# Optimization experiments

Hardware: AMD Instinct MI355X
Metric: run time of the kernel (lower is better)

Reference implementation:

```python
import math
import jax, jax.numpy as jnp
import numpy as np

# ---- static configuration (mirrors init_kwargs / chosen shapes) ----
MUL = 16          # multiplicity in "16x0e+16x1e+16x2e"
B_CFG = 64        # number of configurations in batch
N_ATOM = 64       # atoms per configuration
N_NODES = B_CFG * N_ATOM
N_PAIRS = B_CFG * N_ATOM * N_ATOM

# ---- real Wigner 3j symbols (e3nn convention), computed once in numpy ----
def _su2_cg(j1, m1, j2, m2, j3, m3):
    if m3 != m1 + m2:
        return 0.0
    f = math.factorial
    vmin = max(-j1 + j2 + m3, -j1 + m1, 0)
    vmax = min(j2 + j3 + m1, j3 - j1 + j2, j3 + m3)
    C = math.sqrt((2 * j3 + 1) * f(j3 + j1 - j2) * f(j3 - j1 + j2) * f(j1 + j2 - j3)
                  * f(j3 + m3) * f(j3 - m3)
                  / (f(j1 + j2 + j3 + 1) * f(j1 - m1) * f(j1 + m1) * f(j2 - m2) * f(j2 + m2)))
    S = 0.0
    for v in range(vmin, vmax + 1):
        S += (-1) ** (v + j2 + m2) * f(j2 + j3 + m1 - v) * f(j1 - m1 + v) / (
            f(v) * f(j3 - j1 + j2 - v) * f(j3 + m3 - v) * f(v + j1 - j2 - m3))
    return C * S

def _q_real_to_complex(l):
    q = np.zeros((2 * l + 1, 2 * l + 1), dtype=np.complex128)
    for m in range(-l, 0):
        q[l + m, l + abs(m)] = 1 / 2 ** 0.5
        q[l + m, l - abs(m)] = -1j / 2 ** 0.5
    q[l, l] = 1.0
    for m in range(1, l + 1):
        q[l + m, l + abs(m)] = (-1) ** m / 2 ** 0.5
        q[l + m, l - abs(m)] = 1j * (-1) ** m / 2 ** 0.5
    return (-1j) ** l * q

def _wigner_3j(l1, l2, l3):
    C = np.zeros((2 * l1 + 1, 2 * l2 + 1, 2 * l3 + 1))
    for m1 in range(-l1, l1 + 1):
        for m2 in range(-l2, l2 + 1):
            m3 = m1 + m2
            if abs(m3) <= l3:
                C[l1 + m1, l2 + m2, l3 + m3] = _su2_cg(l1, m1, l2, m2, l3, m3)
    Q1, Q2, Q3 = _q_real_to_complex(l1), _q_real_to_complex(l2), _q_real_to_complex(l3)
    Cr = np.einsum('ij,kl,mn,ikm->jln', Q1, Q2, np.conj(Q3), C.astype(np.complex128))
    assert np.abs(Cr.imag).max() < 1e-6
    Cr = Cr.real
    return Cr / np.linalg.norm(Cr)

# all CG paths (l1, l2, l_out) of the fully connected TP (0e+1e+2e)^2 -> 0e+1e+2e
PATHS = [(0, 0, 0), (1, 1, 0), (2, 2, 0),
         (0, 1, 1), (1, 0, 1), (1, 1, 1), (1, 2, 1), (2, 1, 1), (2, 2, 1),
         (0, 2, 2), (2, 0, 2), (1, 1, 2), (1, 2, 2), (2, 1, 2), (2, 2, 2)]
W3J = {p: _wigner_3j(*p) for p in set(PATHS)}
FAN = {lo: sum(1 for p in PATHS if p[2] == lo) * MUL * MUL for lo in (0, 1, 2)}
ALPHA = {lo: math.sqrt(2 * lo + 1) / math.sqrt(FAN[lo]) for lo in (0, 1, 2)}
# CartesianTensor('ij=ij') change of basis: x_ij = sum_{l,m} QCART[lm,i,j] * irreps[lm]
QCART = np.concatenate([math.sqrt(2 * l + 1) * np.transpose(_wigner_3j(1, 1, l), (2, 0, 1))
                        for l in (0, 1, 2)], axis=0)  # (9, 3, 3), orthonormal rows


def setup_inputs() -> dict:
    key = jax.random.key(0)
    k1, k2 = jax.random.split(key)
    node_feats = jax.random.normal(k1, (N_NODES, MUL * 9), dtype=jnp.float32)
    # layout: for each config, all (i, j) atom pairs with global node indices
    ii, jj = jnp.meshgrid(jnp.arange(N_ATOM, dtype=jnp.int32),
                          jnp.arange(N_ATOM, dtype=jnp.int32), indexing='ij')
    base = (jnp.arange(B_CFG, dtype=jnp.int32) * N_ATOM)[:, None, None]
    rows = (base + ii[None]).reshape(-1)
    cols = (base + jj[None]).reshape(-1)
    layout = jnp.stack([rows, cols], axis=1)  # (N_PAIRS, 2) int32
    tp_weights = jax.random.normal(k2, (len(PATHS), MUL, MUL), dtype=jnp.float32)
    return {'node_feats': node_feats, 'layout': layout, 'tp_weights': tp_weights}


def _split(x):
    # (E, MUL*9) -> {l: (E, MUL, 2l+1)} in irreps order 16x0e | 16x1e | 16x2e
    E = x.shape[0]
    return {0: x[:, :MUL].reshape(E, MUL, 1),
            1: x[:, MUL:4 * MUL].reshape(E, MUL, 3),
            2: x[:, 4 * MUL:].reshape(E, MUL, 5)}


def _forward(node_feats, tp_weights, layout):
    x1 = _split(node_feats[layout[:, 0]])   # gather row atoms
    x2 = _split(node_feats[layout[:, 1]])   # gather column atoms
    E = layout.shape[0]
    dt = node_feats.dtype
    out = {lo: jnp.zeros((E, 2 * lo + 1), dt) for lo in (0, 1, 2)}
    for p, (l1, l2, lo) in enumerate(PATHS):
        w3j = jnp.asarray(W3J[(l1, l2, lo)], dt)
        t = jnp.einsum('eui,uv->evi', x1[l1], tp_weights[p])          # mix multiplicities
        out[lo] = out[lo] + ALPHA[lo] * jnp.einsum('evi,evj,ijk->ek', t, x2[l2], w3j)
    irr = jnp.concatenate([out[0], out[1], out[2]], axis=1)           # (E, 9) = 0e+1e+2e
    cart = jnp.einsum('ek,kij->eij', irr, jnp.asarray(QCART, dt))     # (E, 3, 3)
    # symmetrize: (H + H^T)/2 on the 3n x 3n per-config Hessian
    c = cart.reshape(B_CFG, N_ATOM, N_ATOM, 3, 3)
    c = 0.5 * (c + jnp.transpose(c, (0, 2, 1, 4, 3)))
    return c.reshape(E, 3, 3)


def reference(node_feats, layout, tp_weights):
    return _forward(node_feats, tp_weights, layout)
```

## Files before the change

### kernel.cpp

```cpp
#include <hip/hip_runtime.h>
#include <math.h>


#define NPATH 15

constexpr double cfact(int n){ double r = 1.0; for (int i = 2; i <= n; ++i) r *= (double)i; return r; }
constexpr double csqrt(double x){
  if (x <= 0.0) return 0.0;
  double g = x < 1.0 ? 1.0 : x;
  for (int i = 0; i < 64; ++i) g = 0.5*(g + x/g);
  return g;
}

constexpr double ccg(int j1,int m1,int j2,int m2,int j3,int m3){
  if (m3 != m1 + m2) return 0.0;
  int vmin = -j1 + j2 + m3;
  if (-j1 + m1 > vmin) vmin = -j1 + m1;
  if (0 > vmin) vmin = 0;
  int vmax = j2 + j3 + m1;
  if (j3 - j1 + j2 < vmax) vmax = j3 - j1 + j2;
  if (j3 + m3 < vmax) vmax = j3 + m3;
  double C = csqrt((2.0*j3+1.0)*cfact(j3+j1-j2)*cfact(j3-j1+j2)*cfact(j1+j2-j3)
                   *cfact(j3+m3)*cfact(j3-m3)
                   /(cfact(j1+j2+j3+1)*cfact(j1-m1)*cfact(j1+m1)*cfact(j2-m2)*cfact(j2+m2)));
  double S = 0.0;
  for (int v = vmin; v <= vmax; ++v){
    double term = cfact(j2+j3+m1-v)*cfact(j1-m1+v)
                /(cfact(v)*cfact(j3-j1+j2-v)*cfact(j3+m3-v)*cfact(v+j1-j2-m3));
    S += ((v + j2 + m2) & 1) ? -term : term;
  }
  return C * S;
}

struct QM { double re[5][5]; double im[5][5]; };
constexpr QM cbuild_q(int l){
  QM q{};
  double s = 1.0 / csqrt(2.0);
  for (int m = -l; m < 0; ++m){
    q.re[l+m][l-m] = s;
    q.im[l+m][l+m] = -s;
  }
  q.re[l][l] = 1.0;
  for (int m = 1; m <= l; ++m){
    double sg = (m & 1) ? -1.0 : 1.0;
    q.re[l+m][l+m] = sg * s;
    q.im[l+m][l-m] = sg * s;
  }
  if (l == 1){
    for (int r = 0; r < 5; ++r)
      for (int c = 0; c < 5; ++c){
        double a = q.re[r][c], b = q.im[r][c];
        q.re[r][c] = b; q.im[r][c] = -a;
      }
  } else if (l == 2){
    for (int r = 0; r < 5; ++r)
      for (int c = 0; c < 5; ++c){ q.re[r][c] = -q.re[r][c]; q.im[r][c] = -q.im[r][c]; }
  }
  return q;
}

struct CRP { double v[125]; };
constexpr CRP make_cr(int l1, int l2, int l3){
  QM q1 = cbuild_q(l1), q2 = cbuild_q(l2), q3 = cbuild_q(l3);
  const int d1 = 2*l1+1, d2 = 2*l2+1, d3 = 2*l3+1;
  double CG[125] = {};
  for (int i = 0; i < d1; ++i)
    for (int k = 0; k < d2; ++k)
      for (int m = 0; m < d3; ++m)
        CG[(i*5 + k)*5 + m] = ccg(l1, i-l1, l2, k-l2, l3, m-l3);
  CRP o{};
  for (int j = 0; j < d1; ++j)
    for (int l = 0; l < d2; ++l)
      for (int n = 0; n < d3; ++n){
        double acc = 0.0;
        for (int i = 0; i < d1; ++i)
          for (int k = 0; k < d2; ++k)
            for (int m = 0; m < d3; ++m){
              double c = CG[(i*5 + k)*5 + m];
              if (c == 0.0) continue;
              double are = q1.re[i][j], aim = q1.im[i][j];
              double bre = q2.re[k][l], bim = q2.im[k][l];
              double tre = are*bre - aim*bim;
              double tim = are*bim + aim*bre;
              double cre = q3.re[m][n], cim = q3.im[m][n];
              acc += (tre*cre + tim*cim) * c;
            }
        o.v[(j*d2 + l)*d3 + n] = acc;
      }
  double s2 = 0.0;
  for (int e = 0; e < d1*d2*d3; ++e) s2 += o.v[e]*o.v[e];
  double inv = 1.0 / csqrt(s2);
  for (int e = 0; e < d1*d2*d3; ++e) o.v[e] *= inv;
  return o;
}

constexpr CRP CR0  = make_cr(0,0,0);
constexpr CRP CR1  = make_cr(1,1,0);
constexpr CRP CR2  = make_cr(2,2,0);
constexpr CRP CR3  = make_cr(0,1,1);
constexpr CRP CR4  = make_cr(1,0,1);
constexpr CRP CR5  = make_cr(1,1,1);
constexpr CRP CR6  = make_cr(1,2,1);
constexpr CRP CR7  = make_cr(2,1,1);
constexpr CRP CR8  = make_cr(2,2,1);
constexpr CRP CR9  = make_cr(0,2,2);
constexpr CRP CR10 = make_cr(2,0,2);
constexpr CRP CR11 = make_cr(1,1,2);
constexpr CRP CR12 = make_cr(1,2,2);
constexpr CRP CR13 = make_cr(2,1,2);
constexpr CRP CR14 = make_cr(2,2,2);

struct QCT { double v[81]; };
constexpr QCT make_qc(){
  QCT q{};
  for (int lm = 0; lm < 9; ++lm){
    int l = (lm == 0) ? 0 : ((lm < 4) ? 1 : 2);
    int m = lm - l*l;
    const CRP& cr = (l == 0) ? CR1 : ((l == 1) ? CR5 : CR11);
    double sc = csqrt(2.0*l + 1.0);
    for (int r = 0; r < 9; ++r)
      q.v[lm*9 + r] = cr.v[r*(2*l+1) + m] * sc;
  }
  return q;
}
constexpr QCT QCt = make_qc();

struct WQT { float b8[189*8]; float b1[189]; };
constexpr WQT make_wq(){
  WQT t{};
  const CRP* crs[NPATH] = {&CR0,&CR1,&CR2,&CR3,&CR4,&CR5,&CR6,&CR7,&CR8,&CR9,
                           &CR10,&CR11,&CR12,&CR13,&CR14};
  const int L1[NPATH]   = {0,1,2,0,1,1,1,2,2,0,2,1,1,2,2};
  const int L2[NPATH]   = {0,1,2,1,0,1,2,1,2,2,0,1,2,1,2};
  const int LO[NPATH]   = {0,0,0,1,1,1,1,1,1,2,2,2,2,2,2};
  const int PROW[NPATH] = {0,1,10,35,38,41,50,65,80,105,110,115,124,139,164};
  const double AL[3] = { csqrt(1.0/768.0), csqrt(3.0/1536.0), csqrt(5.0/1536.0) };
  for (int p = 0; p < NPATH; ++p){
    const int d1 = 2*L1[p]+1, d2 = 2*L2[p]+1, d3 = 2*LO[p]+1, lo = LO[p];
    for (int i = 0; i < d1; ++i)
      for (int j = 0; j < d2; ++j)
        for (int a = 0; a < 9; ++a){
          double acc = 0.0;
          for (int m = 0; m < d3; ++m)
            acc += crs[p]->v[(i*d2 + j)*d3 + m] * QCt.v[(lo*lo + m)*9 + a];
          double val = AL[lo] * acc;
          int row = PROW[p] + i*d2 + j;
          if (a < 8) t.b8[row*8 + a] = (float)val;
          else       t.b1[row]       = (float)val;
        }
  }
  return t;
}
__constant__ WQT cWQ = make_wq();

__constant__ int cP_L1[NPATH]   = {0,1,2,0,1,1,1,2,2,0,2,1,1,2,2};
__constant__ int cC2P[51] = {0, 1,1,1, 2,2,2,2,2, 3, 4,4,4, 5,5,5, 6,6,6,
                             7,7,7,7,7, 8,8,8,8,8, 9, 10,10,10,10,10,
                             11,11,11, 12,12,12, 13,13,13,13,13, 14,14,14,14,14};
__constant__ int cC2I[51] = {0, 0,1,2, 0,1,2,3,4, 0, 0,1,2, 0,1,2, 0,1,2,
                             0,1,2,3,4, 0,1,2,3,4, 0, 0,1,2,3,4,
                             0,1,2, 0,1,2, 0,1,2,3,4, 0,1,2,3,4};

#define ACCP(TOFF_, PROW_, D1_)                                              \
  { _Pragma("unroll")                                                        \
    for (int i = 0; i < (D1_); ++i){                                         \
      float tv = pT[((TOFF_) + i) * 16 + v];                                 \
      int row = (PROW_) + i * D2 + j;                                        \
      const float4 m0 = *(const float4*)&sB8[row * 8];                       \
      const float4 m1 = *(const float4*)&sB8[row * 8 + 4];                   \
      const float  m8 = sB1[row];                                            \
      acc[0] += tv*m0.x; acc[1] += tv*m0.y; acc[2] += tv*m0.z;               \
      acc[3] += tv*m0.w; acc[4] += tv*m1.x; acc[5] += tv*m1.y;               \
      acc[6] += tv*m1.z; acc[7] += tv*m1.w; acc[8] += tv*m8;                 \
    } }

__global__ __launch_bounds__(256, 2) void fused2_kernel(
    const float* __restrict__ feats,
    const int*   __restrict__ layout,
    const float* __restrict__ tpw,
    float*       __restrict__ out)
{
  __shared__ __align__(16) float U[11664];
  __shared__ __align__(16) float sMq[4][1728];
  __shared__ __align__(16) float sX1[4][144];
  __shared__ int sCol[64];

  const int tid  = threadIdx.x;
  const int wave = tid >> 6;
  const int lane = tid & 63;
  const int rwBase = blockIdx.x * 4;

  float* sB8  = U;
  float* sB1  = U + 1512;
  float* sTPW = U + 4968;

  for (int o = tid; o < 1512; o += 256) sB8[o] = cWQ.b8[o];
  if (tid < 189) sB1[tid] = cWQ.b1[tid];
  for (int q = tid; q < 960; q += 256)
    *(float4*)&sTPW[q * 4] = ((const float4*)tpw)[q];
  if (tid < 144){
    int w = tid / 36, q = tid - w * 36;
    int rn = layout[2 * ((rwBase + w) * 64)];
    *(float4*)&sX1[w][q * 4] = *(const float4*)(feats + (size_t)rn * 144 + q * 4);
  }
  if (tid >= 192)
    sCol[tid - 192] = layout[2 * ((size_t)rwBase * 64 + (tid - 192)) + 1];
  __syncthreads();

  float* pT = U + 1704 + wave * 816;
  {
    const int v  = lane & 15;
    const int cq = lane >> 4;
    const float* xw = sX1[wave];
    for (int it = 0; it < 13; ++it){
      int c = cq + it * 4;
      if (c < 51){
        int p = cC2P[c], i = cC2I[c];
        int l1 = cP_L1[p];
        int st = 2 * l1 + 1;
        int loff = (l1 == 0) ? 0 : ((l1 == 1) ? 16 : 64);
        const float* xb = xw + loff + i;
        const float* wb = sTPW + p * 256 + v;
        float s = 0.f;
        #pragma unroll
        for (int u = 0; u < 16; ++u) s += xb[u * st] * wb[u * 16];
        pT[c * 16 + v] = s;
      }
    }
  }

  float* pM = sMq[wave];
  for (int rnd = 0; rnd < 3; ++rnd){
    int c = lane + rnd * 64;
    if (c >= 144) break;
    float acc[9];
    #pragma unroll
    for (int a = 0; a < 9; ++a) acc[a] = 0.f;
    if (c < 16){
      const int v = c, j = 0;
      const int D2 = 1;
      ACCP(0,  0,   1)
      ACCP(10, 38,  3)
      ACCP(30, 110, 5)
    } else if (c < 64){
      const int v = (c - 16) / 3, j = (c - 16) % 3;
      const int D2 = 3;
      ACCP(1,  1,   3)
      ACCP(9,  35,  1)
      ACCP(13, 41,  3)
      ACCP(19, 65,  5)
      ACCP(35, 115, 3)
      ACCP(41, 139, 5)
    } else {
      const int v = (c - 64) / 5, j = (c - 64) % 5;
      const int D2 = 5;
      ACCP(4,  10,  5)
      ACCP(16, 50,  3)
      ACCP(24, 80,  5)
      ACCP(29, 105, 1)
      ACCP(38, 124, 3)
      ACCP(46, 164, 5)
    }
    *(float4*)&pM[c * 12]     = make_float4(acc[0], acc[1], acc[2], acc[3]);
    *(float4*)&pM[c * 12 + 4] = make_float4(acc[4], acc[5], acc[6], acc[7]);
    pM[c * 12 + 8] = acc[8];
  }
  __syncthreads();

  float* sX2T = U;
  #pragma unroll
  for (int k = 0; k < 9; ++k){
    int q = k * 256 + tid;
    int j = q / 36, c4 = q - j * 36;
    const float4 xv = *(const float4*)(feats + (size_t)sCol[j] * 144 + c4 * 4);
    int c0 = c4 * 4;
    sX2T[(c0 + 0) * 65 + j] = xv.x;
    sX2T[(c0 + 1) * 65 + j] = xv.y;
    sX2T[(c0 + 2) * 65 + j] = xv.z;
    sX2T[(c0 + 3) * 65 + j] = xv.w;
  }
  __syncthreads();

  float acc[9];
  #pragma unroll
  for (int a = 0; a < 9; ++a) acc[a] = 0.f;

  #pragma unroll 8
  for (int c = 0; c < 144; ++c){
    float x = sX2T[c * 65 + lane];
    const float4 m0 = *(const float4*)&pM[c * 12];
    const float4 m1 = *(const float4*)&pM[c * 12 + 4];
    const float  m8 = pM[c * 12 + 8];
    acc[0] += x * m0.x; acc[1] += x * m0.y; acc[2] += x * m0.z;
    acc[3] += x * m0.w; acc[4] += x * m1.x; acc[5] += x * m1.y;
    acc[6] += x * m1.z; acc[7] += x * m1.w; acc[8] += x * m8;
  }

  float* pO = U + 9360 + wave * 576;
  #pragma unroll
  for (int a = 0; a < 9; ++a) pO[lane * 9 + a] = acc[a];
  float* ob = out + (size_t)(rwBase + wave) * 576;
  #pragma unroll
  for (int r = 0; r < 3; ++r){
    int idx = lane + r * 64;
    if (idx < 144){
      float4 vv = *(const float4*)(pO + idx * 4);
      *(float4*)(ob + idx * 4) = vv;
    }
  }
}

__global__ __launch_bounds__(256) void sym_tiled(float* __restrict__ out){
  __shared__ float sA[16 * 145];
  __shared__ float sB[16 * 145];
  const int tid = threadIdx.x;
  const int b  = blockIdx.x / 10;
  const int tp = blockIdx.x - b * 10;
  const int TI[10] = {0,0,0,0,1,1,1,2,2,3};
  const int TJ[10] = {0,1,2,3,1,2,3,2,3,3};
  const int ti = TI[tp], tj = TJ[tp];
  const bool diag = (ti == tj);
  const size_t cfgBase = (size_t)b * 4096 * 9;

  for (int idx = tid; idx < 2304; idx += 256){
    int r = idx / 144, off = idx - r * 144;
    sA[r * 145 + off] = out[cfgBase + ((size_t)(ti*16 + r) * 64 + tj*16) * 9 + off];
  }
  if (!diag){
    for (int idx = tid; idx < 2304; idx += 256){
      int r = idx / 144, off = idx - r * 144;
      sB[r * 145 + off] = out[cfgBase + ((size_t)(tj*16 + r) * 64 + ti*16) * 9 + off];
    }
  }
  __syncthreads();

  const int di = tid >> 4, dj = tid & 15;
  const float* A = sA;
  const float* B = diag ? sA : sB;
  float oa[9], ob[9];
  #pragma unroll
  for (int a = 0; a < 3; ++a)
    #pragma unroll
    for (int d = 0; d < 3; ++d){
      oa[a*3+d] = 0.5f * (A[di*145 + dj*9 + a*3+d] + B[dj*145 + di*9 + d*3+a]);
      if (!diag)
        ob[a*3+d] = 0.5f * (B[di*145 + dj*9 + a*3+d] + A[dj*145 + di*9 + d*3+a]);
    }
  __syncthreads();

  #pragma unroll
  for (int r9 = 0; r9 < 9; ++r9) sA[di*145 + dj*9 + r9] = oa[r9];
  if (!diag){
    #pragma unroll
    for (int r9 = 0; r9 < 9; ++r9) sB[di*145 + dj*9 + r9] = ob[r9];
  }
  __syncthreads();

  for (int idx = tid; idx < 2304; idx += 256){
    int r = idx / 144, off = idx - r * 144;
    out[cfgBase + ((size_t)(ti*16 + r) * 64 + tj*16) * 9 + off] = sA[r * 145 + off];
  }
  if (!diag){
    for (int idx = tid; idx < 2304; idx += 256){
      int r = idx / 144, off = idx - r * 144;
      out[cfgBase + ((size_t)(tj*16 + r) * 64 + ti*16) * 9 + off] = sB[r * 145 + off];
    }
  }
}

extern "C" void kernel_launch(void* const* d_in, const int* in_sizes, int n_in,
                              void* d_out, int out_size, void* d_ws, size_t ws_size,
                              hipStream_t stream) {
  const float* feats  = (const float*)d_in[0];
  const int*   layout = (const int*)  d_in[1];
  const float* tpw    = (const float*)d_in[2];
  float* out = (float*)d_out;
  (void)d_ws; (void)ws_size; (void)n_in; (void)out_size;

  const int E = in_sizes[1] / 2;
  const int R = E / 64;
  const int B = E / 4096;

  fused2_kernel<<<R / 4, 256, 0, stream>>>(feats, layout, tpw, out);
  sym_tiled<<<B * 10, 256, 0, stream>>>(out);
}
```

Before: 112.5 us.

## Keep per-row Mq in registers, broadcast via readlane, swizzle X2 layout

The per-row contraction matrix Mq is now kept in registers, three chunks per lane, and broadcast across the wave with readlane. It is no longer staged in a per-wave shared-memory buffer. X2 is stored row-major with an XOR swizzle and read as float4 instead of a padded transposed layout. TP weights and X1 are pre-transposed, so the first contraction uses float4 loads and a precomputed metadata table, and occupancy is raised to 3 blocks per SM. This cuts LDS footprint and traffic, but adds many scalar readlane operations and more register pressure.

```diff
diff --git a/kernel.cpp b/kernel.cpp
--- a/kernel.cpp
+++ b/kernel.cpp
@@ -174,132 +174,167 @@
       acc[6] += tv*m1.z; acc[7] += tv*m1.w; acc[8] += tv*m8;                 \
     } }
 
-__global__ __launch_bounds__(256, 2) void fused2_kernel(
+__device__ __forceinline__ void mqc(int c, const float* pT, const float* sB8,
+                                    const float* sB1, float (&acc)[9]){
+  #pragma unroll
+  for (int a = 0; a < 9; ++a) acc[a] = 0.f;
+  if (c < 16){
+    const int v = c, j = 0;
+    const int D2 = 1;
+    ACCP(0,  0,   1)
+    ACCP(10, 38,  3)
+    ACCP(30, 110, 5)
+  } else if (c < 64){
+    const int v = (c - 16) / 3, j = (c - 16) % 3;
+    const int D2 = 3;
+    ACCP(1,  1,   3)
+    ACCP(9,  35,  1)
+    ACCP(13, 41,  3)
+    ACCP(19, 65,  5)
+    ACCP(35, 115, 3)
+    ACCP(41, 139, 5)
+  } else {
+    const int v = (c - 64) / 5, j = (c - 64) % 5;
+    const int D2 = 5;
+    ACCP(4,  10,  5)
+    ACCP(16, 50,  3)
+    ACCP(24, 80,  5)
+    ACCP(29, 105, 1)
+    ACCP(38, 124, 3)
+    ACCP(46, 164, 5)
+  }
+}
+
+__device__ __forceinline__ float rlane(float x, int l){
+  return __int_as_float(__builtin_amdgcn_readlane(__float_as_int(x), l));
+}
+
+#define CCHUNK(MQ_, BASE_) {                                                 \
+  float4 xv = *(const float4*)(xrow + ((c4 ^ lswz) << 2));                   \
+  int l0 = c4 * 4 - (BASE_);                                                 \
+  _Pragma("unroll")                                                          \
+  for (int r = 0; r < 4; ++r){                                               \
+    float xs = (r == 0) ? xv.x : ((r == 1) ? xv.y : ((r == 2) ? xv.z : xv.w)); \
+    acc[0] += xs * rlane(MQ_[0], l0 + r);                                    \
+    acc[1] += xs * rlane(MQ_[1], l0 + r);                                    \
+    acc[2] += xs * rlane(MQ_[2], l0 + r);                                    \
+    acc[3] += xs * rlane(MQ_[3], l0 + r);                                    \
+    acc[4] += xs * rlane(MQ_[4], l0 + r);                                    \
+    acc[5] += xs * rlane(MQ_[5], l0 + r);                                    \
+    acc[6] += xs * rlane(MQ_[6], l0 + r);                                    \
+    acc[7] += xs * rlane(MQ_[7], l0 + r);                                    \
+    acc[8] += xs * rlane(MQ_[8], l0 + r);                                    \
+  } }
+
+__global__ __launch_bounds__(256, 3) void fused3_kernel(
     const float* __restrict__ feats,
     const int*   __restrict__ layout,
     const float* __restrict__ tpw,
     float*       __restrict__ out)
 {
-  __shared__ __align__(16) float U[11664];
-  __shared__ __align__(16) float sMq[4][1728];
-  __shared__ __align__(16) float sX1[4][144];
+  __shared__ __align__(16) float U[11520];
+  __shared__ __align__(16) float sX1T[4][192];
   __shared__ int sCol[64];
+  __shared__ int sMeta[51];
 
   const int tid  = threadIdx.x;
   const int wave = tid >> 6;
   const int lane = tid & 63;
   const int rwBase = blockIdx.x * 4;
-
-  float* sB8  = U;
-  float* sB1  = U + 1512;
-  float* sTPW = U + 4968;
+  const int rw = rwBase + wave;
+
+  float* sB8   = U;
+  float* sB1   = U + 1512;
+  float* sTPWT = U + 4968;
 
   for (int o = tid; o < 1512; o += 256) sB8[o] = cWQ.b8[o];
   if (tid < 189) sB1[tid] = cWQ.b1[tid];
-  for (int q = tid; q < 960; q += 256)
-    *(float4*)&sTPW[q * 4] = ((const float4*)tpw)[q];
-  if (tid < 144){
-    int w = tid / 36, q = tid - w * 36;
-    int rn = layout[2 * ((rwBase + w) * 64)];
-    *(float4*)&sX1[w][q * 4] = *(const float4*)(feats + (size_t)rn * 144 + q * 4);
+  for (int e = tid; e < 3840; e += 256){
+    int p = e >> 8, r = e & 255, u = r >> 4, v = r & 15;
+    sTPWT[p * 324 + v * 20 + u] = tpw[e];
+  }
+  if (tid < 51){
+    int p = cC2P[tid], i = cC2I[tid], l1 = cP_L1[p];
+    int xb = (l1 == 0) ? 0 : ((l1 == 1) ? 16 + i * 20 : 80 + i * 20);
+    sMeta[tid] = xb | ((p * 324) << 16);
   }
   if (tid >= 192)
     sCol[tid - 192] = layout[2 * ((size_t)rwBase * 64 + (tid - 192)) + 1];
+
+  {
+    int rn = layout[2 * (rw * 64)];
+    rn = __builtin_amdgcn_readfirstlane(rn);
+    const float* g = feats + (size_t)rn * 144;
+    float* xt = sX1T[wave];
+    if (lane < 16) xt[lane] = g[lane];
+    if (lane < 48){ int i = lane >> 4, u = lane & 15;
+      xt[16 + i * 20 + u] = g[16 + u * 3 + i]; }
+    { int i = lane >> 4, u = lane & 15;
+      xt[80 + i * 20 + u] = g[64 + u * 5 + i]; }
+    if (lane < 16) xt[160 + lane] = g[64 + lane * 5 + 4];
+  }
   __syncthreads();
 
   float* pT = U + 1704 + wave * 816;
   {
     const int v  = lane & 15;
     const int cq = lane >> 4;
-    const float* xw = sX1[wave];
+    const float* xw = sX1T[wave];
+    #pragma unroll
     for (int it = 0; it < 13; ++it){
       int c = cq + it * 4;
       if (c < 51){
-        int p = cC2P[c], i = cC2I[c];
-        int l1 = cP_L1[p];
-        int st = 2 * l1 + 1;
-        int loff = (l1 == 0) ? 0 : ((l1 == 1) ? 16 : 64);
-        const float* xb = xw + loff + i;
-        const float* wb = sTPW + p * 256 + v;
+        int md = sMeta[c];
+        const float* xb = xw + (md & 0xffff);
+        const float* wb = sTPWT + (md >> 16) + v * 20;
         float s = 0.f;
         #pragma unroll
-        for (int u = 0; u < 16; ++u) s += xb[u * st] * wb[u * 16];
+        for (int u4 = 0; u4 < 4; ++u4){
+          float4 xv = *(const float4*)(xb + u4 * 4);
+          float4 wv = *(const float4*)(wb + u4 * 4);
+          s += xv.x * wv.x; s += xv.y * wv.y;
+          s += xv.z * wv.z; s += xv.w * wv.w;
+        }
         pT[c * 16 + v] = s;
       }
     }
   }
 
-  float* pM = sMq[wave];
-  for (int rnd = 0; rnd < 3; ++rnd){
-    int c = lane + rnd * 64;
-    if (c >= 144) break;
-    float acc[9];
-    #pragma unroll
-    for (int a = 0; a < 9; ++a) acc[a] = 0.f;
-    if (c < 16){
-      const int v = c, j = 0;
-      const int D2 = 1;
-      ACCP(0,  0,   1)
-      ACCP(10, 38,  3)
-      ACCP(30, 110, 5)
-    } else if (c < 64){
-      const int v = (c - 16) / 3, j = (c - 16) % 3;
-      const int D2 = 3;
-      ACCP(1,  1,   3)
-      ACCP(9,  35,  1)
-      ACCP(13, 41,  3)
-      ACCP(19, 65,  5)
-      ACCP(35, 115, 3)
-      ACCP(41, 139, 5)
-    } else {
-      const int v = (c - 64) / 5, j = (c - 64) % 5;
-      const int D2 = 5;
-      ACCP(4,  10,  5)
-      ACCP(16, 50,  3)
-      ACCP(24, 80,  5)
-      ACCP(29, 105, 1)
-      ACCP(38, 124, 3)
-      ACCP(46, 164, 5)
-    }
-    *(float4*)&pM[c * 12]     = make_float4(acc[0], acc[1], acc[2], acc[3]);
-    *(float4*)&pM[c * 12 + 4] = make_float4(acc[4], acc[5], acc[6], acc[7]);
-    pM[c * 12 + 8] = acc[8];
-  }
-  __syncthreads();
-
-  float* sX2T = U;
+  float mq0[9], mq1[9], mq2[9];
+  #pragma unroll
+  for (int a = 0; a < 9; ++a) mq2[a] = 0.f;
+  mqc(lane,       pT, sB8, sB1, mq0);
+  mqc(lane + 64,  pT, sB8, sB1, mq1);
+  if (lane < 16) mqc(lane + 128, pT, sB8, sB1, mq2);
+  __syncthreads();
+
+  float* sX2 = U;
   #pragma unroll
   for (int k = 0; k < 9; ++k){
     int q = k * 256 + tid;
     int j = q / 36, c4 = q - j * 36;
     const float4 xv = *(const float4*)(feats + (size_t)sCol[j] * 144 + c4 * 4);
-    int c0 = c4 * 4;
-    sX2T[(c0 + 0) * 65 + j] = xv.x;
-    sX2T[(c0 + 1) * 65 + j] = xv.y;
-    sX2T[(c0 + 2) * 65 + j] = xv.z;
-    sX2T[(c0 + 3) * 65 + j] = xv.w;
-  }
-  __syncthreads();
-
+    *(float4*)(sX2 + j * 144 + ((c4 ^ (j & 3)) << 2)) = xv;
+  }
+  __syncthreads();
+
+  const float* xrow = sX2 + lane * 144;
+  const int lswz = lane & 3;
   float acc[9];
   #pragma unroll
   for (int a = 0; a < 9; ++a) acc[a] = 0.f;
 
-  #pragma unroll 8
-  for (int c = 0; c < 144; ++c){
-    float x = sX2T[c * 65 + lane];
-    const float4 m0 = *(const float4*)&pM[c * 12];
-    const float4 m1 = *(const float4*)&pM[c * 12 + 4];
-    const float  m8 = pM[c * 12 + 8];
-    acc[0] += x * m0.x; acc[1] += x * m0.y; acc[2] += x * m0.z;
-    acc[3] += x * m0.w; acc[4] += x * m1.x; acc[5] += x * m1.y;
-    acc[6] += x * m1.z; acc[7] += x * m1.w; acc[8] += x * m8;
-  }
-
-  float* pO = U + 9360 + wave * 576;
+  #pragma unroll 2
+  for (int c4 = 0; c4 < 16; ++c4) CCHUNK(mq0, 0)
+  #pragma unroll 2
+  for (int c4 = 16; c4 < 32; ++c4) CCHUNK(mq1, 64)
+  #pragma unroll 2
+  for (int c4 = 32; c4 < 36; ++c4) CCHUNK(mq2, 128)
+
+  float* pO = U + 9216 + wave * 576;
   #pragma unroll
   for (int a = 0; a < 9; ++a) pO[lane * 9 + a] = acc[a];
-  float* ob = out + (size_t)(rwBase + wave) * 576;
+  float* ob = out + (size_t)rw * 576;
   #pragma unroll
   for (int r = 0; r < 3; ++r){
     int idx = lane + r * 64;
@@ -381,6 +416,6 @@
   const int R = E / 64;
   const int B = E / 4096;
 
-  fused2_kernel<<<R / 4, 256, 0, stream>>>(feats, layout, tpw, out);
+  fused3_kernel<<<R / 4, 256, 0, stream>>>(feats, layout, tpw, out);
   sym_tiled<<<B * 10, 256, 0, stream>>>(out);
 }
```

New measurement: 165.9 us. 1.47x slower.

## Stage per-row contraction matrix in global workspace to cut LDS and raise occupancy

Applied to the files above, without the earlier changes.

Adds a new fused kernel that writes each row's 144x9 contraction matrix to a global workspace instead of shared memory, then reads it back through the cache during the final contraction. It also transposes the TP weights and row features in shared memory for float4 dot products, and XOR-swizzles the gathered column features to avoid bank conflicts. The smaller LDS footprint allows three blocks per CU instead of two. The cost is extra global write and read traffic for the matrix, and the old kernel remains as a fallback when the workspace is too small.

```diff
diff --git a/kernel.cpp b/kernel.cpp
--- a/kernel.cpp
+++ b/kernel.cpp
@@ -3,6 +3,8 @@
 
 
 #define NPATH 15
+#define MQ_ROW 12
+#define MQ_STRIDE (144 * MQ_ROW)
 
 constexpr double cfact(int n){ double r = 1.0; for (int i = 2; i <= n; ++i) r *= (double)i; return r; }
 constexpr double csqrt(double x){
@@ -174,6 +176,169 @@
       acc[6] += tv*m1.z; acc[7] += tv*m1.w; acc[8] += tv*m8;                 \
     } }
 
+__global__ __launch_bounds__(256, 3) void fused4_kernel(
+    const float* __restrict__ feats,
+    const int*   __restrict__ layout,
+    const float* __restrict__ tpw,
+    float*       __restrict__ mqg,
+    float*       __restrict__ out)
+{
+  __shared__ __align__(16) float U[11520];
+  __shared__ __align__(16) float sX1T[4][192];
+  __shared__ int sCol[64];
+  __shared__ int sMeta[51];
+
+  const int tid  = threadIdx.x;
+  const int wave = tid >> 6;
+  const int lane = tid & 63;
+  const int rwBase = blockIdx.x * 4;
+  const int rw = rwBase + wave;
+
+  float* sB8   = U;
+  float* sB1   = U + 1512;
+  float* sTPWT = U + 4968;
+
+  for (int o = tid; o < 1512; o += 256) sB8[o] = cWQ.b8[o];
+  if (tid < 189) sB1[tid] = cWQ.b1[tid];
+  for (int e = tid; e < 3840; e += 256){
+    int p = e >> 8, r = e & 255, u = r >> 4, v = r & 15;
+    sTPWT[p * 324 + v * 20 + u] = tpw[e];
+  }
+  if (tid < 51){
+    int p = cC2P[tid], i = cC2I[tid], l1 = cP_L1[p];
+    int xb = (l1 == 0) ? 0 : ((l1 == 1) ? 16 + i * 20 : 80 + i * 20);
+    sMeta[tid] = xb | ((p * 324) << 16);
+  }
+  if (tid >= 192)
+    sCol[tid - 192] = layout[2 * ((size_t)rwBase * 64 + (tid - 192)) + 1];
+
+  {
+    int rn = layout[2 * (rw * 64)];
+    rn = __builtin_amdgcn_readfirstlane(rn);
+    const float* g = feats + (size_t)rn * 144;
+    float* xt = sX1T[wave];
+    if (lane < 16) xt[lane] = g[lane];
+    if (lane < 48){ int i = lane >> 4, u = lane & 15;
+      xt[16 + i * 20 + u] = g[16 + u * 3 + i]; }
+    { int i = lane >> 4, u = lane & 15;
+      xt[80 + i * 20 + u] = g[64 + u * 5 + i]; }
+    if (lane < 16) xt[160 + lane] = g[64 + lane * 5 + 4];
+  }
+  __syncthreads();
+
+  float* pT = U + 1704 + wave * 816;
+  {
+    const int v  = lane & 15;
+    const int cq = lane >> 4;
+    const float* xw = sX1T[wave];
+    #pragma unroll
+    for (int it = 0; it < 13; ++it){
+      int c = cq + it * 4;
+      if (c < 51){
+        int md = sMeta[c];
+        const float* xb = xw + (md & 0xffff);
+        const float* wb = sTPWT + (md >> 16) + v * 20;
+        float s = 0.f;
+        #pragma unroll
+        for (int u4 = 0; u4 < 4; ++u4){
+          float4 xv = *(const float4*)(xb + u4 * 4);
+          float4 wv = *(const float4*)(wb + u4 * 4);
+          s += xv.x * wv.x; s += xv.y * wv.y;
+          s += xv.z * wv.z; s += xv.w * wv.w;
+        }
+        pT[c * 16 + v] = s;
+      }
+    }
+  }
+
+  {
+    float* __restrict__ mqw = mqg + (size_t)rw * MQ_STRIDE;
+    for (int rnd = 0; rnd < 3; ++rnd){
+      int c = lane + rnd * 64;
+      if (c >= 144) break;
+      float acc[9];
+      #pragma unroll
+      for (int a = 0; a < 9; ++a) acc[a] = 0.f;
+      if (c < 16){
+        const int v = c, j = 0;
+        const int D2 = 1;
+        ACCP(0,  0,   1)
+        ACCP(10, 38,  3)
+        ACCP(30, 110, 5)
+      } else if (c < 64){
+        const int v = (c - 16) / 3, j = (c - 16) % 3;
+        const int D2 = 3;
+        ACCP(1,  1,   3)
+        ACCP(9,  35,  1)
+        ACCP(13, 41,  3)
+        ACCP(19, 65,  5)
+        ACCP(35, 115, 3)
+        ACCP(41, 139, 5)
+      } else {
+        const int v = (c - 64) / 5, j = (c - 64) % 5;
+        const int D2 = 5;
+        ACCP(4,  10,  5)
+        ACCP(16, 50,  3)
+        ACCP(24, 80,  5)
+        ACCP(29, 105, 1)
+        ACCP(38, 124, 3)
+        ACCP(46, 164, 5)
+      }
+      *(float4*)(mqw + c * MQ_ROW)     = make_float4(acc[0], acc[1], acc[2], acc[3]);
+      *(float4*)(mqw + c * MQ_ROW + 4) = make_float4(acc[4], acc[5], acc[6], acc[7]);
+      mqw[c * MQ_ROW + 8] = acc[8];
+    }
+  }
+  __syncthreads();
+
+  float* sX2 = U;
+  #pragma unroll
+  for (int k = 0; k < 9; ++k){
+    int q = k * 256 + tid;
+    int j = q / 36, c4 = q - j * 36;
+    const float4 xv = *(const float4*)(feats + (size_t)sCol[j] * 144 + c4 * 4);
+    *(float4*)(sX2 + j * 144 + ((c4 ^ (j & 3)) << 2)) = xv;
+  }
+  __syncthreads();
+
+  const float* mqr = mqg + (size_t)rw * MQ_STRIDE;
+  asm volatile("" : "+v"(mqr));
+  const float* xrow = sX2 + lane * 144;
+  const int lswz = lane & 3;
+  float acc[9];
+  #pragma unroll
+  for (int a = 0; a < 9; ++a) acc[a] = 0.f;
+
+  #pragma unroll 4
+  for (int c4 = 0; c4 < 36; ++c4){
+    float4 xv = *(const float4*)(xrow + ((c4 ^ lswz) << 2));
+    #pragma unroll
+    for (int r = 0; r < 4; ++r){
+      int c = c4 * 4 + r;
+      float xs = (r == 0) ? xv.x : ((r == 1) ? xv.y : ((r == 2) ? xv.z : xv.w));
+      const float4 m0 = *(const float4*)(mqr + c * MQ_ROW);
+      const float4 m1 = *(const float4*)(mqr + c * MQ_ROW + 4);
+      const float  m8 = *(mqr + c * MQ_ROW + 8);
+      acc[0] += xs * m0.x; acc[1] += xs * m0.y; acc[2] += xs * m0.z;
+      acc[3] += xs * m0.w; acc[4] += xs * m1.x; acc[5] += xs * m1.y;
+      acc[6] += xs * m1.z; acc[7] += xs * m1.w; acc[8] += xs * m8;
+    }
+  }
+
+  float* pO = U + 9216 + wave * 576;
+  #pragma unroll
+  for (int a = 0; a < 9; ++a) pO[lane * 9 + a] = acc[a];
+  float* ob = out + (size_t)rw * 576;
+  #pragma unroll
+  for (int r = 0; r < 3; ++r){
+    int idx = lane + r * 64;
+    if (idx < 144){
+      float4 vv = *(const float4*)(pO + idx * 4);
+      *(float4*)(ob + idx * 4) = vv;
+    }
+  }
+}
+
 __global__ __launch_bounds__(256, 2) void fused2_kernel(
     const float* __restrict__ feats,
     const int*   __restrict__ layout,
@@ -296,7 +461,7 @@
     acc[6] += x * m1.z; acc[7] += x * m1.w; acc[8] += x * m8;
   }
 
-  float* pO = U + 9360 + wave * 576;
+  float* pO = U + 9216 + wave * 576;
   #pragma unroll
   for (int a = 0; a < 9; ++a) pO[lane * 9 + a] = acc[a];
   float* ob = out + (size_t)(rwBase + wave) * 576;
@@ -375,12 +540,18 @@
   const int*   layout = (const int*)  d_in[1];
   const float* tpw    = (const float*)d_in[2];
   float* out = (float*)d_out;
-  (void)d_ws; (void)ws_size; (void)n_in; (void)out_size;
+  float* ws  = (float*)d_ws;
+  (void)n_in; (void)out_size;
 
   const int E = in_sizes[1] / 2;
   const int R = E / 64;
   const int B = E / 4096;
 
-  fused2_kernel<<<R / 4, 256, 0, stream>>>(feats, layout, tpw, out);
+  const size_t need = (size_t)R * MQ_STRIDE * sizeof(float);
+  if (ws_size >= need){
+    fused4_kernel<<<R / 4, 256, 0, stream>>>(feats, layout, tpw, ws, out);
+  } else {
+    fused2_kernel<<<R / 4, 256, 0, stream>>>(feats, layout, tpw, out);
+  }
   sym_tiled<<<B * 10, 256, 0, stream>>>(out);
 }
```

New measurement: 194.0 us. 1.72x slower.
